# Performance work log

Hardware: AMD Instinct MI355X
Metric: run time of the kernel (lower is better)

Reference implementation:

```python
import jax, jax.numpy as jnp
import numpy as np

N_NODES = 50000
N_EDGES = 800000
N_GRAPHS = 64
D = 64            # input_dim == hidden_dim == output_dim
N_GIN = 4         # num_layers - 1 GINConv layers
N_PRED = 5        # num_layers prediction heads
BN_EPS = 1e-5


def setup_inputs() -> dict:
    key = jax.random.key(0)
    ks = jax.random.split(key, 12)
    x = jax.random.normal(ks[0], (N_NODES, D), dtype=jnp.float32)
    edge_index = jax.random.randint(ks[1], (2, N_EDGES), 0, N_NODES, dtype=jnp.int32)
    # contiguous graph ids covering all N_GRAPHS segments (PyG batch vector)
    batch = ((jnp.arange(N_NODES) * N_GRAPHS) // N_NODES).astype(jnp.int32)
    s = 1.0 / np.sqrt(D)
    mlp_W1 = jax.random.uniform(ks[2], (N_GIN, D, D), jnp.float32, -s, s)
    mlp_b1 = jax.random.uniform(ks[3], (N_GIN, D), jnp.float32, -s, s)
    mlp_W2 = jax.random.uniform(ks[4], (N_GIN, D, D), jnp.float32, -s, s)
    mlp_b2 = jax.random.uniform(ks[5], (N_GIN, D), jnp.float32, -s, s)
    bn_gamma = jnp.ones((N_GIN, D), jnp.float32)
    bn_beta = jnp.zeros((N_GIN, D), jnp.float32)
    prelu_alpha = jnp.float32(0.25)  # nn.PReLU default, shared across layers
    pred_W = jax.random.uniform(ks[6], (N_PRED, D, D), jnp.float32, -s, s)
    pred_b = jax.random.uniform(ks[7], (N_PRED, D), jnp.float32, -s, s)
    return {
        "x": x, "edge_index": edge_index, "batch": batch,
        "mlp_W1": mlp_W1, "mlp_b1": mlp_b1, "mlp_W2": mlp_W2, "mlp_b2": mlp_b2,
        "bn_gamma": bn_gamma, "bn_beta": bn_beta, "prelu_alpha": prelu_alpha,
        "pred_W": pred_W, "pred_b": pred_b,
    }


def reference(x, edge_index, batch, mlp_W1, mlp_b1, mlp_W2, mlp_b2,
              bn_gamma, bn_beta, prelu_alpha, pred_W, pred_b):
    src, dst = edge_index[0], edge_index[1]
    h = x
    hidden_rep = [h]
    for l in range(N_GIN):
        # GINConv, eps = 0 (learn_eps=False): (1+eps)*x_i + sum_{j->i} x_j
        agg = jax.ops.segment_sum(h[src], dst, num_segments=N_NODES)
        z = h + agg
        # 2-layer MLP: Linear -> ReLU -> Linear
        z = jax.nn.relu(z @ mlp_W1[l] + mlp_b1[l])
        z = z @ mlp_W2[l] + mlp_b2[l]
        # BatchNorm1d over nodes (training-mode batch stats)
        mean = z.mean(axis=0)
        var = z.var(axis=0)
        z = (z - mean) * jax.lax.rsqrt(var + BN_EPS) * bn_gamma[l] + bn_beta[l]
        # shared single-parameter PReLU
        h = jnp.where(z > 0, z, prelu_alpha * z)
        hidden_rep.append(h)
    # per-layer max graph pooling + linear head (dropout_prob=0 -> identity)
    reps = []
    for l, hr in enumerate(hidden_rep):
        pooled = jax.ops.segment_max(hr, batch, num_segments=N_GRAPHS)
        reps.append(pooled @ pred_W[l] + pred_b[l])
    # torch.stack(dim=-1) -> (B, D, L), 'cat' aggregation flattens to (B, D*L)
    return jnp.stack(reps, axis=-1).reshape(N_GRAPHS, -1)
```

## Files before the change

### kernel.cpp

```cpp
#include <hip/hip_runtime.h>
#include <hip/hip_bf16.h>

#define N_NODES 50000
#define N_EDGES 800000
#define N_GRAPHS 64
#define DIM 64
#define N_GIN 4
#define N_PRED 5
#define BN_EPS 1e-5f
#define MM_BLOCKS 782
#define PART_ROWS 391
#define NB 625
#define BUCKET_SZ 80

typedef short bf16x8 __attribute__((ext_vector_type(8)));
typedef float f32x4 __attribute__((ext_vector_type(4)));

__device__ __forceinline__ float b2f(__hip_bfloat16 v) { return __bfloat162float(v); }

__device__ __forceinline__ float loadv(const void* p, size_t i, int isb) {
    return isb ? b2f(((const __hip_bfloat16*)p)[i]) : ((const float*)p)[i];
}

__device__ __forceinline__ unsigned short f2bu(float f) {
    __hip_bfloat16 h = __float2bfloat16(f);
    return *(unsigned short*)&h;
}
__device__ __forceinline__ float bu2f(unsigned short u) {
    __hip_bfloat16 h = *(__hip_bfloat16*)&u;
    return b2f(h);
}

__device__ __forceinline__ unsigned int enc_f(float f) {
    unsigned int b = __float_as_uint(f);
    return (b & 0x80000000u) ? ~b : (b | 0x80000000u);
}
__device__ __forceinline__ float dec_f(unsigned int u) {
    unsigned int b = (u & 0x80000000u) ? (u ^ 0x80000000u) : ~u;
    return __uint_as_float(b);
}

__device__ __forceinline__ unsigned int gstart(unsigned int g) {
    return (g * (unsigned int)N_NODES + (N_GRAPHS - 1)) >> 6;
}

__global__ void detect_dtype(const unsigned int* __restrict__ xw, int* __restrict__ flag) {
    __shared__ int cnt[256];
    int t = threadIdx.x;
    int c = 0;
    for (int i = t; i < 1024; i += 256) {
        unsigned int e = (xw[i] >> 7) & 0xFFu;
        if (e >= 0x70u && e <= 0x85u) c++;
    }
    cnt[t] = c;
    __syncthreads();
    for (int s = 128; s > 0; s >>= 1) {
        if (t < s) cnt[t] += cnt[t + s];
        __syncthreads();
    }
    if (t == 0) *flag = (cnt[0] >= 512) ? 1 : 0;
}

__global__ void zero_u32(unsigned int* __restrict__ p, int n) {
    int i = blockIdx.x * blockDim.x + threadIdx.x;
    if (i < n) p[i] = 0u;
}

__global__ __launch_bounds__(256) void convert_pool_bg(
    const void* __restrict__ x, unsigned short* __restrict__ H,
    unsigned int* __restrict__ poolEnc, const int* __restrict__ dflag) {
    __shared__ float shmx[4][64];
    int isb = *dflag;
    unsigned int g = blockIdx.x >> 2, p = blockIdx.x & 3;
    unsigned int s = gstart(g), e = gstart(g + 1), len = e - s;
    unsigned int rs = s + (len * p) / 4, re = s + (len * (p + 1)) / 4;
    int r = threadIdx.x >> 6, c = threadIdx.x & 63;
    float mx = -3.0e38f;
    for (unsigned int row = rs + r; row < re; row += 4) {
        float v = loadv(x, (size_t)row * DIM + c, isb);
        H[(size_t)row * DIM + c] = f2bu(v);
        mx = fmaxf(mx, v);
    }
    shmx[r][c] = mx;
    __syncthreads();
    if (threadIdx.x < 64) {
        float m = fmaxf(fmaxf(shmx[0][c], shmx[1][c]), fmaxf(shmx[2][c], shmx[3][c]));
        atomicMax(&poolEnc[g * DIM + c], enc_f(m));
    }
}


__global__ __launch_bounds__(256) void bucket_hist(const int* __restrict__ dst,
                                                   unsigned int* __restrict__ bucketCnt) {
    __shared__ unsigned int h[NB];
    for (int i = threadIdx.x; i < NB; i += 256) h[i] = 0u;
    __syncthreads();
    for (int e = blockIdx.x * 256 + threadIdx.x; e < N_EDGES; e += gridDim.x * 256)
        atomicAdd(&h[(unsigned int)dst[e] / BUCKET_SZ], 1u);
    __syncthreads();
    for (int i = threadIdx.x; i < NB; i += 256) {
        unsigned int v = h[i];
        if (v) atomicAdd(&bucketCnt[i], v);
    }
}

__global__ void scan_buckets(const unsigned int* __restrict__ bucketCnt,
                             unsigned int* __restrict__ bucketBase,
                             unsigned int* __restrict__ bucketCur) {
    __shared__ unsigned int s[256];
    int t = threadIdx.x;
    int i0 = t * 3;
    unsigned int v0 = (i0 < NB) ? bucketCnt[i0] : 0u;
    unsigned int v1 = (i0 + 1 < NB) ? bucketCnt[i0 + 1] : 0u;
    unsigned int v2 = (i0 + 2 < NB) ? bucketCnt[i0 + 2] : 0u;
    unsigned int tsum = v0 + v1 + v2;
    s[t] = tsum;
    __syncthreads();
    for (int off = 1; off < 256; off <<= 1) {
        unsigned int u = (t >= off) ? s[t - off] : 0u;
        __syncthreads();
        s[t] += u;
        __syncthreads();
    }
    unsigned int ex = s[t] - tsum;
    if (i0 < NB)     { bucketBase[i0] = ex;          bucketCur[i0] = ex; }
    if (i0 + 1 < NB) { bucketBase[i0 + 1] = ex + v0; bucketCur[i0 + 1] = ex + v0; }
    if (i0 + 2 < NB) { bucketBase[i0 + 2] = ex + v0 + v1; bucketCur[i0 + 2] = ex + v0 + v1; }
}

__global__ __launch_bounds__(256) void bucket_scatter(
    const int* __restrict__ src, const int* __restrict__ dst,
    unsigned int* __restrict__ bucketCur, uint2* __restrict__ ebuf) {
    __shared__ unsigned int h[NB];
    __shared__ unsigned int base[NB];
    for (int i = threadIdx.x; i < NB; i += 256) h[i] = 0u;
    __syncthreads();
    for (int e = blockIdx.x * 256 + threadIdx.x; e < N_EDGES; e += gridDim.x * 256)
        atomicAdd(&h[(unsigned int)dst[e] / BUCKET_SZ], 1u);
    __syncthreads();
    for (int i = threadIdx.x; i < NB; i += 256) {
        unsigned int v = h[i];
        base[i] = v ? atomicAdd(&bucketCur[i], v) : 0u;
        h[i] = 0u;
    }
    __syncthreads();
    for (int e = blockIdx.x * 256 + threadIdx.x; e < N_EDGES; e += gridDim.x * 256) {
        unsigned int d = (unsigned int)dst[e];
        unsigned int b = d / BUCKET_SZ;
        unsigned int off = atomicAdd(&h[b], 1u);
        ebuf[base[b] + off] = make_uint2((unsigned int)src[e], d);
    }
}

__global__ __launch_bounds__(256) void bucket_csr(
    const uint2* __restrict__ ebuf, const unsigned int* __restrict__ bucketBase,
    const unsigned int* __restrict__ bucketCnt, unsigned int* __restrict__ deg,
    unsigned int* __restrict__ cur, unsigned int* __restrict__ srclist) {
    __shared__ unsigned int ldeg[BUCKET_SZ], lcur[BUCKET_SZ], lscan[BUCKET_SZ];
    int b = blockIdx.x;
    unsigned int ebase = bucketBase[b];
    unsigned int ecnt = bucketCnt[b];
    unsigned int nbase = (unsigned int)b * BUCKET_SZ;
    int t = threadIdx.x;
    if (t < BUCKET_SZ) ldeg[t] = 0u;
    __syncthreads();
    for (unsigned int i = t; i < ecnt; i += 256)
        atomicAdd(&ldeg[ebuf[ebase + i].y - nbase], 1u);
    __syncthreads();
    if (t < BUCKET_SZ) lscan[t] = ldeg[t];
    __syncthreads();
    for (int off = 1; off < BUCKET_SZ; off <<= 1) {
        unsigned int u = 0u;
        if (t < BUCKET_SZ && t >= off) u = lscan[t - off];
        __syncthreads();
        if (t < BUCKET_SZ) lscan[t] += u;
        __syncthreads();
    }
    if (t < BUCKET_SZ) {
        lcur[t] = lscan[t] - ldeg[t];
        deg[nbase + t] = ldeg[t];
        cur[nbase + t] = ebase + lscan[t];
    }
    __syncthreads();
    for (unsigned int i = t; i < ecnt; i += 256) {
        uint2 e = ebuf[ebase + i];
        unsigned int off = atomicAdd(&lcur[e.y - nbase], 1u);
        srclist[ebase + off] = e.x;
    }
}


__global__ void pack_w(const void* __restrict__ W1, const void* __restrict__ W2,
                       unsigned short* __restrict__ P, const int* __restrict__ dflag) {
    int isb = *dflag;
    int mi = blockIdx.x;
    const void* src = (mi < 4) ? W1 : W2;
    size_t off = (size_t)(mi & 3) * 4096;
    for (int it = 0; it < 16; it++) {
        int idx = it * 256 + threadIdx.x;
        int j = idx & 7, l = (idx >> 3) & 63, s = (idx >> 9) & 1, t = idx >> 10;
        int k = s * 32 + (l >> 4) * 8 + j;
        int n = t * 16 + (l & 15);
        P[(size_t)mi * 4096 + idx] = f2bu(loadv(src, off + (size_t)k * 64 + n, isb));
    }
}

__global__ __launch_bounds__(256) void gather_agg8(
    const unsigned short* __restrict__ H, unsigned short* __restrict__ Xb,
    const unsigned int* __restrict__ cur, const unsigned int* __restrict__ deg,
    const unsigned int* __restrict__ srclist) {
    int lane = threadIdx.x & 63;
    int w = threadIdx.x >> 6;
    int node = blockIdx.x * 4 + w;
    int g8 = lane >> 3;
    int t8 = lane & 7;
    unsigned int cnt = deg[node];
    unsigned int start = cur[node] - cnt;
    const unsigned int* sl = srclist + start;
    float a[8] = {0.f, 0.f, 0.f, 0.f, 0.f, 0.f, 0.f, 0.f};
    if (g8 == 0) {
        bf16x8 sv = *(const bf16x8*)&H[(size_t)node * DIM + t8 * 8];
#pragma unroll
        for (int k = 0; k < 8; k++) a[k] = bu2f((unsigned short)sv[k]);
    }
    for (unsigned int j = g8; j < cnt; j += 8) {
        unsigned int s = sl[j];
        bf16x8 v = *(const bf16x8*)&H[(size_t)s * DIM + t8 * 8];
#pragma unroll
        for (int k = 0; k < 8; k++) a[k] += bu2f((unsigned short)v[k]);
    }
#pragma unroll
    for (int k = 0; k < 8; k++) {
        a[k] += __shfl_xor(a[k], 8);
        a[k] += __shfl_xor(a[k], 16);
        a[k] += __shfl_xor(a[k], 32);
    }
    if (g8 == 0) {
        bf16x8 o;
#pragma unroll
        for (int k = 0; k < 8; k++) o[k] = (short)f2bu(a[k]);
        *(bf16x8*)&Xb[(size_t)node * DIM + t8 * 8] = o;
    }
}

__global__ __launch_bounds__(256) void fused_mm(
    const unsigned short* __restrict__ Xb,
    const unsigned short* __restrict__ P1, const unsigned short* __restrict__ P2,
    const void* __restrict__ b1, size_t b1Off, const void* __restrict__ b2, size_t b2Off,
    float* __restrict__ Zf, float* __restrict__ part, const int* __restrict__ dflag) {
    __shared__ __align__(16) short T2[4][16][72];
    __shared__ float S1[4][64], S2[4][64];
    int isb = *dflag;
    int tid = threadIdx.x;
    int lane = tid & 63;
    int w = tid >> 6;
    int r0 = blockIdx.x * 64 + w * 16;
    bool valid = (r0 < N_NODES);
    int m = lane & 15, q = lane >> 4;
    int row = valid ? (r0 + m) : m;

    const bf16x8* Xv = (const bf16x8*)Xb;
    bf16x8 a0 = Xv[(size_t)row * 8 + q];
    bf16x8 a1 = Xv[(size_t)row * 8 + 4 + q];
    const bf16x8* P1v = (const bf16x8*)P1;
    const bf16x8* P2v = (const bf16x8*)P2;
    bf16x8 w1[8], w2[8];
#pragma unroll
    for (int i = 0; i < 8; i++) {
        w1[i] = P1v[(size_t)i * 64 + lane];
        w2[i] = P2v[(size_t)i * 64 + lane];
    }

    f32x4 acc[4] = {{0.f, 0.f, 0.f, 0.f}, {0.f, 0.f, 0.f, 0.f},
                    {0.f, 0.f, 0.f, 0.f}, {0.f, 0.f, 0.f, 0.f}};
#pragma unroll
    for (int t = 0; t < 4; t++) {
        acc[t] = __builtin_amdgcn_mfma_f32_16x16x32_bf16(a0, w1[t * 2 + 0], acc[t], 0, 0, 0);
        acc[t] = __builtin_amdgcn_mfma_f32_16x16x32_bf16(a1, w1[t * 2 + 1], acc[t], 0, 0, 0);
    }
#pragma unroll
    for (int t = 0; t < 4; t++) {
        int col = t * 16 + m;
        float bv = loadv(b1, b1Off + col, isb);
#pragma unroll
        for (int reg = 0; reg < 4; reg++) {
            float v = acc[t][reg] + bv;
            v = v > 0.0f ? v : 0.0f;
            T2[w][q * 4 + reg][col] = (short)f2bu(v);
        }
    }

    bf16x8 c0 = *(const bf16x8*)&T2[w][m][q * 8];
    bf16x8 c1 = *(const bf16x8*)&T2[w][m][32 + q * 8];
    f32x4 acc2[4] = {{0.f, 0.f, 0.f, 0.f}, {0.f, 0.f, 0.f, 0.f},
                     {0.f, 0.f, 0.f, 0.f}, {0.f, 0.f, 0.f, 0.f}};
#pragma unroll
    for (int t = 0; t < 4; t++) {
        acc2[t] = __builtin_amdgcn_mfma_f32_16x16x32_bf16(c0, w2[t * 2 + 0], acc2[t], 0, 0, 0);
        acc2[t] = __builtin_amdgcn_mfma_f32_16x16x32_bf16(c1, w2[t * 2 + 1], acc2[t], 0, 0, 0);
    }

    float s1[4], s2[4];
#pragma unroll
    for (int t = 0; t < 4; t++) {
        float a = 0.0f, b = 0.0f;
        if (valid) {
            int col = t * 16 + m;
            float bv = loadv(b2, b2Off + col, isb);
            int rbase = r0 + q * 4;
#pragma unroll
            for (int reg = 0; reg < 4; reg++) {
                float z = acc2[t][reg] + bv;
                Zf[(size_t)(rbase + reg) * DIM + col] = z;
                a += z;
                b += z * z;
            }
        }
        s1[t] = a;
        s2[t] = b;
    }
#pragma unroll
    for (int t = 0; t < 4; t++) {
        s1[t] += __shfl_xor(s1[t], 16);
        s1[t] += __shfl_xor(s1[t], 32);
        s2[t] += __shfl_xor(s2[t], 16);
        s2[t] += __shfl_xor(s2[t], 32);
    }
    if (q == 0) {
#pragma unroll
        for (int t = 0; t < 4; t++) {
            S1[w][t * 16 + m] = s1[t];
            S2[w][t * 16 + m] = s2[t];
        }
    }
    __syncthreads();
    if (tid < 128) {
        int c = tid & 63;
        float v = (tid < 64) ? (S1[0][c] + S1[1][c] + S1[2][c] + S1[3][c])
                             : (S2[0][c] + S2[1][c] + S2[2][c] + S2[3][c]);
        atomicAdd(&part[(size_t)(blockIdx.x >> 1) * 128 + tid], v);
    }
}

__global__ void stats_finalize(const float* __restrict__ part,
                               const void* __restrict__ gamma, const void* __restrict__ beta,
                               size_t gOff, float* __restrict__ scsh,
                               const int* __restrict__ dflag) {
    __shared__ double sh1[256], sh2[256];
    int c = blockIdx.x;
    int t = threadIdx.x;
    double a1 = 0.0, a2 = 0.0;
    for (int b = t; b < PART_ROWS; b += 256) {
        a1 += (double)part[(size_t)b * 128 + c];
        a2 += (double)part[(size_t)b * 128 + 64 + c];
    }
    sh1[t] = a1;
    sh2[t] = a2;
    __syncthreads();
    for (int s = 128; s > 0; s >>= 1) {
        if (t < s) { sh1[t] += sh1[t + s]; sh2[t] += sh2[t + s]; }
        __syncthreads();
    }
    if (t == 0) {
        int isb = *dflag;
        double mean = sh1[0] * (1.0 / N_NODES);
        double var = sh2[0] * (1.0 / N_NODES) - mean * mean;
        float inv = rsqrtf(fmaxf((float)var, 0.0f) + BN_EPS);
        float g = loadv(gamma, gOff + c, isb);
        float bb = loadv(beta, gOff + c, isb);
        scsh[c] = g * inv;
        scsh[64 + c] = bb - (float)mean * g * inv;
    }
}

__global__ __launch_bounds__(256) void bn_prelu_pool_bg(
    const float* __restrict__ Z, unsigned short* __restrict__ H,
    const float* __restrict__ scsh, const void* __restrict__ alpha_p,
    unsigned int* __restrict__ poolEnc, const int* __restrict__ dflag) {
    __shared__ float shmx[4][64];
    int isb = *dflag;
    float alpha = loadv(alpha_p, 0, isb);
    unsigned int g = blockIdx.x >> 2, p = blockIdx.x & 3;
    unsigned int s = gstart(g), e = gstart(g + 1), len = e - s;
    unsigned int rs = s + (len * p) / 4, re = s + (len * (p + 1)) / 4;
    int r = threadIdx.x >> 6, c = threadIdx.x & 63;
    float sc = scsh[c], sh = scsh[64 + c];
    float mx = -3.0e38f;
    for (unsigned int row = rs + r; row < re; row += 4) {
        float v = Z[(size_t)row * DIM + c] * sc + sh;
        v = v > 0.0f ? v : alpha * v;
        H[(size_t)row * DIM + c] = f2bu(v);
        mx = fmaxf(mx, v);
    }
    shmx[r][c] = mx;
    __syncthreads();
    if (threadIdx.x < 64) {
        float m = fmaxf(fmaxf(shmx[0][c], shmx[1][c]), fmaxf(shmx[2][c], shmx[3][c]));
        atomicMax(&poolEnc[g * DIM + c], enc_f(m));
    }
}


__global__ void convert_pool_f(const void* __restrict__ x, float* __restrict__ A,
                               const int* __restrict__ batch,
                               unsigned int* __restrict__ poolEnc,
                               const int* __restrict__ dflag) {
    int isb = *dflag;
    int idx = blockIdx.x * blockDim.x + threadIdx.x;
    if (idx >= N_NODES * DIM) return;
    int i = idx >> 6, c = idx & 63;
    float v = loadv(x, idx, isb);
    A[idx] = v;
    atomicMax(&poolEnc[batch[i] * DIM + c], enc_f(v));
}

__global__ void copy_f4(const float4* __restrict__ A, float4* __restrict__ B, int n4) {
    int i = blockIdx.x * blockDim.x + threadIdx.x;
    if (i < n4) B[i] = A[i];
}

__global__ void edge_scatter(const int* __restrict__ src, const int* __restrict__ dst,
                             const float* __restrict__ A, float* __restrict__ B) {
    int idx = blockIdx.x * blockDim.x + threadIdx.x;
    if (idx >= N_EDGES * 16) return;
    int e = idx >> 4, q = idx & 15;
    int s = src[e], d = dst[e];
    float4 v = ((const float4*)(A + (size_t)s * DIM))[q];
    float* bp = B + (size_t)d * DIM + (q << 2);
    atomicAdd(bp + 0, v.x);
    atomicAdd(bp + 1, v.y);
    atomicAdd(bp + 2, v.z);
    atomicAdd(bp + 3, v.w);
}

template <bool RELU, bool STATS>
__global__ void mm64(const float* __restrict__ X, const void* __restrict__ W, size_t wOff,
                     const void* __restrict__ bias, size_t bOff, float* __restrict__ Y,
                     double* __restrict__ stats, const int* __restrict__ dflag) {
    int isb = *dflag;
    __shared__ float Ws[64][64];
    __shared__ float Xs[4][64];
    __shared__ float Sv[4][64];
    __shared__ float bsh[64];
    int tid = threadIdx.x;
    for (int i = tid; i < 4096; i += 256) Ws[i >> 6][i & 63] = loadv(W, wOff + i, isb);
    if (tid < 64) bsh[tid] = loadv(bias, bOff + tid, isb);
    int r = tid >> 6, d = tid & 63;
    int row = blockIdx.x * 4 + r;
    Xs[r][d] = X[(size_t)row * DIM + d];
    __syncthreads();
    float acc = bsh[d];
#pragma unroll
    for (int k = 0; k < 64; k++) acc += Xs[r][k] * Ws[k][d];
    if (RELU) acc = acc > 0.0f ? acc : 0.0f;
    Y[(size_t)row * DIM + d] = acc;
    if (STATS) {
        Sv[r][d] = acc;
        __syncthreads();
        if (tid < 64) {
            float s = 0.0f, s2 = 0.0f;
#pragma unroll
            for (int rr = 0; rr < 4; rr++) {
                float v = Sv[rr][tid];
                s += v;
                s2 += v * v;
            }
            atomicAdd(&stats[tid], (double)s);
            atomicAdd(&stats[64 + tid], (double)s2);
        }
    }
}

__global__ void bn_prelu_pool_f(const float* __restrict__ Z, float* __restrict__ H,
                                const double* __restrict__ stats,
                                const void* __restrict__ gamma, const void* __restrict__ beta,
                                size_t gOff, const void* __restrict__ alpha_p,
                                const int* __restrict__ batch,
                                unsigned int* __restrict__ poolEnc,
                                const int* __restrict__ dflag) {
    int isb = *dflag;
    int idx = blockIdx.x * blockDim.x + threadIdx.x;
    if (idx >= N_NODES * DIM) return;
    int i = idx >> 6, c = idx & 63;
    double mn = stats[c] * (1.0 / N_NODES);
    double var = stats[64 + c] * (1.0 / N_NODES) - mn * mn;
    float inv = rsqrtf(fmaxf((float)var, 0.0f) + BN_EPS);
    float z = Z[idx];
    float v = (z - (float)mn) * inv * loadv(gamma, gOff + c, isb) + loadv(beta, gOff + c, isb);
    float alpha = loadv(alpha_p, 0, isb);
    v = v > 0.0f ? v : alpha * v;
    H[idx] = v;
    atomicMax(&poolEnc[batch[i] * DIM + c], enc_f(v));
}

__global__ void pred_head(const unsigned int* __restrict__ poolEnc,
                          const void* __restrict__ predW, const void* __restrict__ predB,
                          void* __restrict__ out, const int* __restrict__ dflag) {
    int isb = *dflag;
    int l = blockIdx.x / N_GRAPHS;
    int g = blockIdx.x % N_GRAPHS;
    int d = threadIdx.x;
    __shared__ float ps[64];
    ps[d] = dec_f(poolEnc[(size_t)l * N_GRAPHS * DIM + g * DIM + d]);
    __syncthreads();
    float acc = loadv(predB, (size_t)l * DIM + d, isb);
    size_t wbase = (size_t)l * DIM * DIM;
#pragma unroll
    for (int k = 0; k < 64; k++) acc += ps[k] * loadv(predW, wbase + k * DIM + d, isb);
    int o = g * (DIM * N_PRED) + d * N_PRED + l;
    if (isb) ((__hip_bfloat16*)out)[o] = __float2bfloat16(acc);
    else ((float*)out)[o] = acc;
}

extern "C" void kernel_launch(void* const* d_in, const int* in_sizes, int n_in,
                              void* d_out, int out_size, void* d_ws, size_t ws_size,
                              hipStream_t stream) {
    const void* x     = d_in[0];
    const int*  edge  = (const int*)d_in[1];
    const int*  batch = (const int*)d_in[2];
    const void* W1    = d_in[3];
    const void* b1    = d_in[4];
    const void* W2    = d_in[5];
    const void* b2    = d_in[6];
    const void* gamma = d_in[7];
    const void* beta  = d_in[8];
    const void* alpha = d_in[9];
    const void* pW    = d_in[10];
    const void* pB    = d_in[11];

    float* A = (float*)d_ws;
    float* B = A + (size_t)N_NODES * DIM;
    double* statsF = (double*)(B + (size_t)N_NODES * DIM);
    unsigned int* poolEnc   = (unsigned int*)(statsF + 128);
    unsigned int* bucketCnt = poolEnc + N_PRED * N_GRAPHS * DIM;
    int* dflag = (int*)(bucketCnt + NB);
    unsigned int* deg        = (unsigned int*)(dflag + 1);
    unsigned int* cur        = deg + N_NODES;
    unsigned int* bucketBase = cur + N_NODES;
    unsigned int* bucketCur  = bucketBase + NB;
    unsigned int* srclist    = bucketCur + NB;
    unsigned short* Wpack = (unsigned short*)(srclist + N_EDGES);
    float* part = (float*)(Wpack + 8 * 4096);
    float* scsh = part + (size_t)PART_ROWS * 128;
    uint2* ebuf = (uint2*)B;

    size_t needFull = (size_t)((char*)(scsh + 128) - (char*)d_ws);
    bool useMFMA = ws_size >= needFull;

    const int* esrc = edge;
    const int* edst = edge + N_EDGES;
    const int ND = N_NODES * DIM;

    unsigned short* Hb = (unsigned short*)A;
    unsigned short* Xb = Hb + (size_t)N_NODES * DIM;
    float* Zf = B;

    detect_dtype<<<1, 256, 0, stream>>>((const unsigned int*)x, dflag);
    zero_u32<<<(N_PRED * N_GRAPHS * DIM + NB + 255) / 256, 256, 0, stream>>>(
        poolEnc, N_PRED * N_GRAPHS * DIM + NB);

    if (useMFMA) {
        bucket_hist<<<200, 256, 0, stream>>>(edst, bucketCnt);
        scan_buckets<<<1, 256, 0, stream>>>(bucketCnt, bucketBase, bucketCur);
        bucket_scatter<<<200, 256, 0, stream>>>(esrc, edst, bucketCur, ebuf);
        bucket_csr<<<NB, 256, 0, stream>>>(ebuf, bucketBase, bucketCnt, deg, cur, srclist);

        pack_w<<<8, 256, 0, stream>>>(W1, W2, Wpack, dflag);
        convert_pool_bg<<<N_GRAPHS * 4, 256, 0, stream>>>(x, Hb, poolEnc, dflag);
        const int PN = PART_ROWS * 128;
        for (int l = 0; l < N_GIN; l++) {
            size_t bOff = (size_t)l * DIM;
            gather_agg8<<<N_NODES / 4, 256, 0, stream>>>(Hb, Xb, cur, deg, srclist);
            zero_u32<<<(PN + 255) / 256, 256, 0, stream>>>((unsigned int*)part, PN);
            fused_mm<<<MM_BLOCKS, 256, 0, stream>>>(
                Xb, Wpack + (size_t)l * 4096, Wpack + (size_t)(4 + l) * 4096,
                b1, bOff, b2, bOff, Zf, part, dflag);
            stats_finalize<<<64, 256, 0, stream>>>(part, gamma, beta, bOff, scsh, dflag);
            bn_prelu_pool_bg<<<N_GRAPHS * 4, 256, 0, stream>>>(
                Zf, Hb, scsh, alpha, poolEnc + (size_t)(l + 1) * N_GRAPHS * DIM, dflag);
        }
    } else {
        convert_pool_f<<<ND / 256, 256, 0, stream>>>(x, A, batch, poolEnc, dflag);
        for (int l = 0; l < N_GIN; l++) {
            size_t wOff = (size_t)l * DIM * DIM;
            size_t bOff = (size_t)l * DIM;
            copy_f4<<<(ND / 4 + 255) / 256, 256, 0, stream>>>((const float4*)A, (float4*)B,
                                                              ND / 4);
            edge_scatter<<<(N_EDGES * 16) / 256, 256, 0, stream>>>(esrc, edst, A, B);
            mm64<true, false><<<N_NODES / 4, 256, 0, stream>>>(B, W1, wOff, b1, bOff, A, nullptr,
                                                               dflag);
            zero_u32<<<1, 256, 0, stream>>>((unsigned int*)statsF, 256);
            mm64<false, true><<<N_NODES / 4, 256, 0, stream>>>(A, W2, wOff, b2, bOff, B, statsF,
                                                               dflag);
            bn_prelu_pool_f<<<ND / 256, 256, 0, stream>>>(
                B, A, statsF, gamma, beta, bOff, alpha, batch,
                poolEnc + (size_t)(l + 1) * N_GRAPHS * DIM, dflag);
        }
    }
    pred_head<<<N_PRED * N_GRAPHS, DIM, 0, stream>>>(poolEnc, pW, pB, d_out, dflag);
}
```

Baseline: 372.6 us.

## Store pre-BN activations in bf16, drop partial-stat atomics, widen pooling grid

The fused MLP kernel now writes its pre-BatchNorm output as bf16 instead of fp32, which halves the intermediate traffic read back by the BN/PReLU/pool kernel. Per-block statistics are written directly to a per-block row rather than atomically added into shared rows, which removes the per-layer zeroing kernel. The pooling kernels are launched with 16 blocks per graph instead of 4 to raise parallelism. Rounding Z to bf16 before normalization adds some precision loss.

```diff
diff --git a/kernel.cpp b/kernel.cpp
--- a/kernel.cpp
+++ b/kernel.cpp
@@ -9,9 +9,9 @@
 #define N_PRED 5
 #define BN_EPS 1e-5f
 #define MM_BLOCKS 782
-#define PART_ROWS 391
 #define NB 625
 #define BUCKET_SZ 80
+#define POOL_CH 16
 
 typedef short bf16x8 __attribute__((ext_vector_type(8)));
 typedef float f32x4 __attribute__((ext_vector_type(4)));
@@ -71,9 +71,9 @@
     unsigned int* __restrict__ poolEnc, const int* __restrict__ dflag) {
     __shared__ float shmx[4][64];
     int isb = *dflag;
-    unsigned int g = blockIdx.x >> 2, p = blockIdx.x & 3;
+    unsigned int g = blockIdx.x / POOL_CH, p = blockIdx.x % POOL_CH;
     unsigned int s = gstart(g), e = gstart(g + 1), len = e - s;
-    unsigned int rs = s + (len * p) / 4, re = s + (len * (p + 1)) / 4;
+    unsigned int rs = s + (len * p) / POOL_CH, re = s + (len * (p + 1)) / POOL_CH;
     int r = threadIdx.x >> 6, c = threadIdx.x & 63;
     float mx = -3.0e38f;
     for (unsigned int row = rs + r; row < re; row += 4) {
@@ -247,7 +247,8 @@
     const unsigned short* __restrict__ Xb,
     const unsigned short* __restrict__ P1, const unsigned short* __restrict__ P2,
     const void* __restrict__ b1, size_t b1Off, const void* __restrict__ b2, size_t b2Off,
-    float* __restrict__ Zf, float* __restrict__ part, const int* __restrict__ dflag) {
+    unsigned short* __restrict__ Zb, float* __restrict__ part,
+    const int* __restrict__ dflag) {
     __shared__ __align__(16) short T2[4][16][72];
     __shared__ float S1[4][64], S2[4][64];
     int isb = *dflag;
@@ -311,7 +312,7 @@
 #pragma unroll
             for (int reg = 0; reg < 4; reg++) {
                 float z = acc2[t][reg] + bv;
-                Zf[(size_t)(rbase + reg) * DIM + col] = z;
+                Zb[(size_t)(rbase + reg) * DIM + col] = f2bu(z);
                 a += z;
                 b += z * z;
             }
@@ -338,7 +339,7 @@
         int c = tid & 63;
         float v = (tid < 64) ? (S1[0][c] + S1[1][c] + S1[2][c] + S1[3][c])
                              : (S2[0][c] + S2[1][c] + S2[2][c] + S2[3][c]);
-        atomicAdd(&part[(size_t)(blockIdx.x >> 1) * 128 + tid], v);
+        part[(size_t)blockIdx.x * 128 + tid] = v;
     }
 }
 
@@ -350,7 +351,7 @@
     int c = blockIdx.x;
     int t = threadIdx.x;
     double a1 = 0.0, a2 = 0.0;
-    for (int b = t; b < PART_ROWS; b += 256) {
+    for (int b = t; b < MM_BLOCKS; b += 256) {
         a1 += (double)part[(size_t)b * 128 + c];
         a2 += (double)part[(size_t)b * 128 + 64 + c];
     }
@@ -374,20 +375,20 @@
 }
 
 __global__ __launch_bounds__(256) void bn_prelu_pool_bg(
-    const float* __restrict__ Z, unsigned short* __restrict__ H,
+    const unsigned short* __restrict__ Zb, unsigned short* __restrict__ H,
     const float* __restrict__ scsh, const void* __restrict__ alpha_p,
     unsigned int* __restrict__ poolEnc, const int* __restrict__ dflag) {
     __shared__ float shmx[4][64];
     int isb = *dflag;
     float alpha = loadv(alpha_p, 0, isb);
-    unsigned int g = blockIdx.x >> 2, p = blockIdx.x & 3;
+    unsigned int g = blockIdx.x / POOL_CH, p = blockIdx.x % POOL_CH;
     unsigned int s = gstart(g), e = gstart(g + 1), len = e - s;
-    unsigned int rs = s + (len * p) / 4, re = s + (len * (p + 1)) / 4;
+    unsigned int rs = s + (len * p) / POOL_CH, re = s + (len * (p + 1)) / POOL_CH;
     int r = threadIdx.x >> 6, c = threadIdx.x & 63;
     float sc = scsh[c], sh = scsh[64 + c];
     float mx = -3.0e38f;
     for (unsigned int row = rs + r; row < re; row += 4) {
-        float v = Z[(size_t)row * DIM + c] * sc + sh;
+        float v = bu2f(Zb[(size_t)row * DIM + c]) * sc + sh;
         v = v > 0.0f ? v : alpha * v;
         H[(size_t)row * DIM + c] = f2bu(v);
         mx = fmaxf(mx, v);
@@ -541,7 +542,7 @@
     unsigned int* srclist    = bucketCur + NB;
     unsigned short* Wpack = (unsigned short*)(srclist + N_EDGES);
     float* part = (float*)(Wpack + 8 * 4096);
-    float* scsh = part + (size_t)PART_ROWS * 128;
+    float* scsh = part + (size_t)MM_BLOCKS * 128;
     uint2* ebuf = (uint2*)B;
 
     size_t needFull = (size_t)((char*)(scsh + 128) - (char*)d_ws);
@@ -553,7 +554,7 @@
 
     unsigned short* Hb = (unsigned short*)A;
     unsigned short* Xb = Hb + (size_t)N_NODES * DIM;
-    float* Zf = B;
+    unsigned short* Zb = (unsigned short*)B;
 
     detect_dtype<<<1, 256, 0, stream>>>((const unsigned int*)x, dflag);
     zero_u32<<<(N_PRED * N_GRAPHS * DIM + NB + 255) / 256, 256, 0, stream>>>(
@@ -566,18 +567,16 @@
         bucket_csr<<<NB, 256, 0, stream>>>(ebuf, bucketBase, bucketCnt, deg, cur, srclist);
 
         pack_w<<<8, 256, 0, stream>>>(W1, W2, Wpack, dflag);
-        convert_pool_bg<<<N_GRAPHS * 4, 256, 0, stream>>>(x, Hb, poolEnc, dflag);
-        const int PN = PART_ROWS * 128;
+        convert_pool_bg<<<N_GRAPHS * POOL_CH, 256, 0, stream>>>(x, Hb, poolEnc, dflag);
         for (int l = 0; l < N_GIN; l++) {
             size_t bOff = (size_t)l * DIM;
             gather_agg8<<<N_NODES / 4, 256, 0, stream>>>(Hb, Xb, cur, deg, srclist);
-            zero_u32<<<(PN + 255) / 256, 256, 0, stream>>>((unsigned int*)part, PN);
             fused_mm<<<MM_BLOCKS, 256, 0, stream>>>(
                 Xb, Wpack + (size_t)l * 4096, Wpack + (size_t)(4 + l) * 4096,
-                b1, bOff, b2, bOff, Zf, part, dflag);
+                b1, bOff, b2, bOff, Zb, part, dflag);
             stats_finalize<<<64, 256, 0, stream>>>(part, gamma, beta, bOff, scsh, dflag);
-            bn_prelu_pool_bg<<<N_GRAPHS * 4, 256, 0, stream>>>(
-                Zf, Hb, scsh, alpha, poolEnc + (size_t)(l + 1) * N_GRAPHS * DIM, dflag);
+            bn_prelu_pool_bg<<<N_GRAPHS * POOL_CH, 256, 0, stream>>>(
+                Zb, Hb, scsh, alpha, poolEnc + (size_t)(l + 1) * N_GRAPHS * DIM, dflag);
         }
     } else {
         convert_pool_f<<<ND / 256, 256, 0, stream>>>(x, A, batch, poolEnc, dflag);
```

Result: faster. 324.2 us (-13.0%).
